# Kernel tuning notes

Hardware: AMD Instinct MI355X
Metric: run time of the kernel (lower is better)

## Reference

```python
import jax, jax.numpy as jnp
import numpy as np

N = 10000      # nodes
E = 65536      # edges
IN = 16        # in_channels
H = 64         # hidden_channels
ED = 4         # edge_attr_dim
MLP_H = 64     # hidden width of edge-weight MLPs


def _glorot(key, shape):
    fan_in, fan_out = shape[0], shape[1]
    lim = np.sqrt(6.0 / (fan_in + fan_out)).astype(np.float32)
    return jax.random.uniform(key, shape, jnp.float32, -lim, lim)


def setup_inputs() -> dict:
    key = jax.random.key(0)
    ks = jax.random.split(key, 16)
    x = jax.random.normal(ks[0], (N, IN), dtype=jnp.float32)
    edge_index = jax.random.randint(ks[1], (2, E), 0, N, dtype=jnp.int64)
    edge_attr = jax.random.normal(ks[2], (E, ED), dtype=jnp.float32)
    return {
        "x": x,
        "edge_index": edge_index,
        "edge_attr": edge_attr,
        # nn1: Linear(ED,64) -> ReLU -> Linear(64, IN*H)
        "nn1_w1": _glorot(ks[3], (ED, MLP_H)), "nn1_b1": jnp.zeros((MLP_H,), jnp.float32),
        "nn1_w2": _glorot(ks[4], (MLP_H, IN * H)), "nn1_b2": jnp.zeros((IN * H,), jnp.float32),
        "root1": _glorot(ks[5], (IN, H)), "bias1": jnp.zeros((H,), jnp.float32),
        # nn2: Linear(ED,64) -> ReLU -> Linear(64, H*H)
        "nn2_w1": _glorot(ks[6], (ED, MLP_H)), "nn2_b1": jnp.zeros((MLP_H,), jnp.float32),
        "nn2_w2": _glorot(ks[7], (MLP_H, H * H)), "nn2_b2": jnp.zeros((H * H,), jnp.float32),
        "root2": _glorot(ks[8], (H, H)), "bias2": jnp.zeros((H,), jnp.float32),
        # readout MLP
        "lin1_w": _glorot(ks[9], (H, 8)), "lin1_b": jnp.zeros((8,), jnp.float32),
        "lin2_w": _glorot(ks[10], (8, 1)), "lin2_b": jnp.zeros((1,), jnp.float32),
    }


def _nnconv(x, src, dst, edge_attr, w1, b1, w2, b2, root, bias, cin, cout):
    # Edge-conditioned weight generation: MLP(edge_attr) -> [E, cin, cout]
    h = jax.nn.relu(edge_attr @ w1 + b1)
    We = (h @ w2 + b2).reshape(-1, cin, cout)
    # Per-edge matmul: message_e = x[src_e] @ We_e  -> [E, cout]
    msg = jnp.einsum('ei,eio->eo', x[src], We)
    # Scatter mean over destination nodes
    s = jax.ops.segment_sum(msg, dst, num_segments=N)
    cnt = jax.ops.segment_sum(jnp.ones((msg.shape[0],), x.dtype), dst, num_segments=N)
    agg = s / jnp.maximum(cnt, 1.0)[:, None]
    # Root transform + bias (PyG NNConv defaults: root_weight=True, bias=True)
    return agg + x @ root + bias


def reference(x, edge_index, edge_attr,
              nn1_w1, nn1_b1, nn1_w2, nn1_b2, root1, bias1,
              nn2_w1, nn2_b1, nn2_w2, nn2_b2, root2, bias2,
              lin1_w, lin1_b, lin2_w, lin2_b):
    # Dropout layers are identity in eval mode.
    src, dst = edge_index[0], edge_index[1]
    h = jax.nn.relu(_nnconv(x, src, dst, edge_attr,
                            nn1_w1, nn1_b1, nn1_w2, nn1_b2, root1, bias1, IN, H))
    h = jax.nn.relu(_nnconv(h, src, dst, edge_attr,
                            nn2_w1, nn2_b1, nn2_w2, nn2_b2, root2, bias2, H, H))
    h = jax.nn.relu(h @ lin1_w + lin1_b)
    return (h @ lin2_w + lin2_b)[:, 0]  # squeeze(-1) -> [N]
```

## Files before the change

kernel.cpp:

```cpp
#include <hip/hip_runtime.h>
#include <hip/hip_bf16.h>

#define NN 10000
#define EE 65536

using short8  = __attribute__((ext_vector_type(8))) short;
using u16x8   = __attribute__((ext_vector_type(8))) unsigned short;
using float4v = __attribute__((ext_vector_type(4))) float;

__device__ __forceinline__ unsigned short f2b(float f){
  union { float f; unsigned int u; } v; v.f = f;
  unsigned int u = v.u;
  unsigned int r = (u + 0x7fff + ((u >> 16) & 1)) >> 16;
  return (unsigned short)r;
}


__device__ __forceinline__ void do_permB(int idx, const float* __restrict__ w2,
                                         unsigned short* __restrict__ Bt, int cin){
  int K = cin*64;
  int o = idx / K;
  int k = idx - o*K;
  int m = k / cin;
  int i = k - m*cin;
  Bt[idx] = f2b(w2[(size_t)m*(cin*64) + i*64 + o]);
}

__global__ __launch_bounds__(256) void k_prep(
    const float* __restrict__ w2a, unsigned short* __restrict__ Bt1,
    const float* __restrict__ w2b, unsigned short* __restrict__ Bt2,
    int* __restrict__ cnt){
  int b = blockIdx.x;
  int t = threadIdx.x;
  if(b < 40){
    int i = b*256 + t;
    if(i < NN) cnt[i] = 0;
  } else if(b < 296){
    do_permB((b-40)*256 + t, w2a, Bt1, 16);
  } else {
    do_permB((b-296)*256 + t, w2b, Bt2, 64);
  }
}


__global__ void k_hist(const int* __restrict__ dst, int* __restrict__ cnt){
  int e = blockIdx.x*256 + threadIdx.x;
  if(e < EE) atomicAdd(&cnt[dst[e]], 1);
}

__global__ __launch_bounds__(1024) void k_scan(const int* __restrict__ cnt, int* __restrict__ offs, int* __restrict__ cursor){
  const int T = 1024, PER = (NN + T - 1)/T;
  int tid = threadIdx.x;
  int base = tid*PER;
  int local[PER];
  int s = 0;
  #pragma unroll
  for(int j=0;j<PER;j++){
    int i = base+j;
    int v = (i<NN)? cnt[i] : 0;
    local[j] = s;
    s += v;
  }
  int lane = tid & 63, wv = tid >> 6;
  int val = s;
  #pragma unroll
  for(int o=1;o<64;o<<=1){
    int u = __shfl_up(val, o, 64);
    if(lane >= o) val += u;
  }
  __shared__ int wsum[16];
  if(lane==63) wsum[wv] = val;
  __syncthreads();
  if(tid==0){
    int acc=0;
    #pragma unroll
    for(int i=0;i<16;i++){ int t2=wsum[i]; wsum[i]=acc; acc+=t2; }
  }
  __syncthreads();
  int thr_excl = wsum[wv] + (val - s);
  #pragma unroll
  for(int j=0;j<PER;j++){
    int i = base+j;
    if(i<NN){ int e = thr_excl + local[j]; offs[i]=e; cursor[i]=e; }
  }
  if(tid == T-1) offs[NN] = thr_excl + s;
}

__global__ void k_scatter(const int* __restrict__ dst, const int* __restrict__ src,
                          int* __restrict__ cursor, int2* __restrict__ elist2){
  int e = blockIdx.x*256 + threadIdx.x;
  if(e < EE){ int p = atomicAdd(&cursor[dst[e]], 1); elist2[p] = make_int2(e, src[e]); }
}


__global__ __launch_bounds__(64) void k_accK1(const float* __restrict__ x,
    const int* __restrict__ offs, const int2* __restrict__ elist2,
    const float* __restrict__ ea, const float* __restrict__ w1, const float* __restrict__ b1,
    unsigned short* __restrict__ K1, float* __restrict__ XS, int v0){
  int v = v0 + blockIdx.x;
  int L = threadIdx.x;
  int cg = L & 3, mg = L >> 2;
  int i0 = cg << 2;
  float w1c0 = w1[L], w1c1 = w1[64+L], w1c2 = w1[128+L], w1c3 = w1[192+L];
  float b1c = b1[L];
  __shared__ float sh[2][64];
  float acc[4][4];
  #pragma unroll
  for(int j=0;j<4;j++)
    #pragma unroll
    for(int c=0;c<4;c++) acc[j][c]=0.f;
  float4 xs = make_float4(0.f,0.f,0.f,0.f);
  int p0 = offs[v], p1 = offs[v+1];
  float4 a_nxt = make_float4(0.f,0.f,0.f,0.f);
  float4 x_nxt = make_float4(0.f,0.f,0.f,0.f);
  if(p0 < p1){
    int2 es = elist2[p0];
    a_nxt = *(const float4*)(ea + (size_t)es.x*4);
    x_nxt = *(const float4*)(x + (size_t)es.y*16 + i0);
  }
  for(int p=p0;p<p1;p++){
    int buf = (p-p0)&1;
    float4 xv = x_nxt;
    float4 av = a_nxt;
    float hv = fmaxf(b1c + av.x*w1c0 + av.y*w1c1 + av.z*w1c2 + av.w*w1c3, 0.f);
    sh[buf][L] = hv;
    __syncthreads();
    if(p+1<p1){
      int2 es = elist2[p+1];
      a_nxt = *(const float4*)(ea + (size_t)es.x*4);
      x_nxt = *(const float4*)(x + (size_t)es.y*16 + i0);
    }
    xs.x += xv.x; xs.y += xv.y; xs.z += xv.z; xs.w += xv.w;
    #pragma unroll
    for(int j=0;j<4;j++){
      float hm = sh[buf][mg + 16*j];
      acc[j][0] += hm*xv.x; acc[j][1] += hm*xv.y;
      acc[j][2] += hm*xv.z; acc[j][3] += hm*xv.w;
    }
  }
  unsigned short* Kv = K1 + (size_t)blockIdx.x*1024;
  #pragma unroll
  for(int j=0;j<4;j++){
    int m = mg + 16*j;
    ushort4 u;
    u.x=f2b(acc[j][0]); u.y=f2b(acc[j][1]); u.z=f2b(acc[j][2]); u.w=f2b(acc[j][3]);
    *(ushort4*)(Kv + m*16 + i0) = u;
  }
  if(mg==0) *(float4*)(XS + (size_t)v*64 + i0) = xs;
}


__global__ __launch_bounds__(64) void k_accK2(const float* __restrict__ x1,
    const int* __restrict__ offs, const int2* __restrict__ elist2,
    const float* __restrict__ ea, const float* __restrict__ w1, const float* __restrict__ b1,
    unsigned short* __restrict__ K, float* __restrict__ XS, int v0){
  int v = v0 + blockIdx.x;
  int L = threadIdx.x;
  int cg = L & 7, mg = L >> 3;
  int i0 = cg << 3;
  float w1c0 = w1[L], w1c1 = w1[64+L], w1c2 = w1[128+L], w1c3 = w1[192+L];
  float b1c = b1[L];
  __shared__ float sh[2][64];
  float acc[8][8];
  #pragma unroll
  for(int j=0;j<8;j++)
    #pragma unroll
    for(int c=0;c<8;c++) acc[j][c]=0.f;
  float4 xs0 = make_float4(0.f,0.f,0.f,0.f);
  float4 xs1 = make_float4(0.f,0.f,0.f,0.f);
  int p0 = offs[v], p1 = offs[v+1];
  float4 a_nxt = make_float4(0.f,0.f,0.f,0.f);
  float4 x_nxt0 = make_float4(0.f,0.f,0.f,0.f);
  float4 x_nxt1 = make_float4(0.f,0.f,0.f,0.f);
  if(p0 < p1){
    int2 es = elist2[p0];
    a_nxt = *(const float4*)(ea + (size_t)es.x*4);
    const float* xr = x1 + (size_t)es.y*64 + i0;
    x_nxt0 = *(const float4*)xr;
    x_nxt1 = *(const float4*)(xr+4);
  }
  for(int p=p0;p<p1;p++){
    int buf = (p-p0)&1;
    float4 xv0 = x_nxt0, xv1 = x_nxt1;
    float4 av = a_nxt;
    float hv = fmaxf(b1c + av.x*w1c0 + av.y*w1c1 + av.z*w1c2 + av.w*w1c3, 0.f);
    sh[buf][L] = hv;
    __syncthreads();
    if(p+1<p1){
      int2 es = elist2[p+1];
      a_nxt = *(const float4*)(ea + (size_t)es.x*4);
      const float* xr = x1 + (size_t)es.y*64 + i0;
      x_nxt0 = *(const float4*)xr;
      x_nxt1 = *(const float4*)(xr+4);
    }
    xs0.x += xv0.x; xs0.y += xv0.y; xs0.z += xv0.z; xs0.w += xv0.w;
    xs1.x += xv1.x; xs1.y += xv1.y; xs1.z += xv1.z; xs1.w += xv1.w;
    float4 h4a = *(float4*)&sh[buf][mg*8];
    float4 h4b = *(float4*)&sh[buf][mg*8+4];
    #pragma unroll
    for(int jj=0;jj<2;jj++){
      float4 h4 = jj? h4b : h4a;
      #pragma unroll
      for(int tq=0;tq<4;tq++){
        int j = jj*4+tq;
        float hm = (tq==0)?h4.x:(tq==1)?h4.y:(tq==2)?h4.z:h4.w;
        acc[j][0] += hm*xv0.x; acc[j][1] += hm*xv0.y;
        acc[j][2] += hm*xv0.z; acc[j][3] += hm*xv0.w;
        acc[j][4] += hm*xv1.x; acc[j][5] += hm*xv1.y;
        acc[j][6] += hm*xv1.z; acc[j][7] += hm*xv1.w;
      }
    }
  }
  unsigned short* Kv = K + (size_t)blockIdx.x*4096;
  #pragma unroll
  for(int j=0;j<8;j++){
    int m = mg*8 + j;
    u16x8 u;
    #pragma unroll
    for(int c=0;c<8;c++) u[c] = f2b(acc[j][c]);
    *(u16x8*)(Kv + m*64 + i0) = u;
  }
  if(mg==0){
    *(float4*)(XS + (size_t)v*64 + i0)     = xs0;
    *(float4*)(XS + (size_t)v*64 + i0 + 4) = xs1;
  }
}


#define GBK 64

__global__ __launch_bounds__(256) void k_gemm(const unsigned short* __restrict__ A,
    const unsigned short* __restrict__ Bt, float* __restrict__ P,
    int rows, int Ktot, int Kc){
  __shared__ unsigned short As[64*72];
  __shared__ unsigned short Bs[64*72];
  int t = threadIdx.x;
  int lane = t & 63;
  int w = t >> 6;
  int row0 = blockIdx.x*64;
  int k0 = blockIdx.y*Kc;

  int srow  = t >> 3;
  int skseg = (t & 7) << 3;

  float4v acc[4];
  #pragma unroll
  for(int ct=0;ct<4;ct++)
    #pragma unroll
    for(int qq=0;qq<4;qq++) acc[ct][qq]=0.f;

  int lrow = lane & 15;
  int lk   = (lane >> 4) << 3;

  short8 a_pf[2], b_pf[2];
  int T = Kc/GBK;

  {
    int kk = k0 + skseg;
    #pragma unroll
    for(int qq=0;qq<2;qq++){
      int gr = row0 + srow + 32*qq;
      short8 z = {0,0,0,0,0,0,0,0};
      a_pf[qq] = (gr<rows)? *(const short8*)(A + (size_t)gr*Ktot + kk) : z;
      int o = srow + 32*qq;
      b_pf[qq] = *(const short8*)(Bt + (size_t)o*Ktot + kk);
    }
  }

  for(int tt=0; tt<T; tt++){
    __syncthreads();
    #pragma unroll
    for(int qq=0;qq<2;qq++){
      *(short8*)(As + (srow + 32*qq)*72 + skseg) = a_pf[qq];
      *(short8*)(Bs + (srow + 32*qq)*72 + skseg) = b_pf[qq];
    }
    __syncthreads();
    if(tt+1 < T){
      int kk = k0 + (tt+1)*GBK + skseg;
      #pragma unroll
      for(int qq=0;qq<2;qq++){
        int gr = row0 + srow + 32*qq;
        short8 z = {0,0,0,0,0,0,0,0};
        a_pf[qq] = (gr<rows)? *(const short8*)(A + (size_t)gr*Ktot + kk) : z;
        int o = srow + 32*qq;
        b_pf[qq] = *(const short8*)(Bt + (size_t)o*Ktot + kk);
      }
    }
    #pragma unroll
    for(int k32=0;k32<2;k32++){
      int kf = k32*32 + lk;
      short8 a0 = *(short8*)(As + (w*16 + lrow)*72 + kf);
      #pragma unroll
      for(int ct=0;ct<4;ct++){
        short8 b = *(short8*)(Bs + (ct*16 + lrow)*72 + kf);
        acc[ct] = __builtin_amdgcn_mfma_f32_16x16x32_bf16(a0, b, acc[ct], 0,0,0);
      }
    }
  }
  size_t base = (size_t)blockIdx.y*rows*64;
  int quad = lane >> 4;
  #pragma unroll
  for(int ct=0;ct<4;ct++){
    int c = ct*16 + lrow;
    #pragma unroll
    for(int reg=0;reg<4;reg++){
      int r = row0 + w*16 + quad*4 + reg;
      if(r < rows) P[base + (size_t)r*64 + c] = acc[ct][reg];
    }
  }
}


template<int CIN, int SPLIT>
__global__ __launch_bounds__(256) void k_reduce_ep(const float* __restrict__ P, int rows, int v0,
    const float* __restrict__ XS, const float* __restrict__ b2, const float* __restrict__ xprev,
    const float* __restrict__ root, const float* __restrict__ bias, const int* __restrict__ offs,
    float* __restrict__ out){
  int idx = blockIdx.x*256 + threadIdx.x;
  if(idx >= rows*16) return;
  int r = idx >> 4, og = (idx & 15) << 2;
  int v = v0 + r;

  float4 s = make_float4(0.f,0.f,0.f,0.f);
  #pragma unroll
  for(int z=0; z<SPLIT; z++){
    float4 p = *(const float4*)(P + ((size_t)z*rows + r)*64 + og);
    s.x += p.x; s.y += p.y; s.z += p.z; s.w += p.w;
  }
  #pragma unroll
  for(int i=0;i<CIN;i++){
    float xsv = XS[(size_t)v*64 + i];
    float4 b = *(const float4*)(b2 + i*64 + og);
    s.x += xsv*b.x; s.y += xsv*b.y; s.z += xsv*b.z; s.w += xsv*b.w;
  }
  float4 rt = make_float4(0.f,0.f,0.f,0.f);
  #pragma unroll
  for(int i=0;i<CIN;i++){
    float xv = xprev[(size_t)v*CIN + i];
    float4 wv = *(const float4*)(root + i*64 + og);
    rt.x += xv*wv.x; rt.y += xv*wv.y; rt.z += xv*wv.z; rt.w += xv*wv.w;
  }
  float c = (float)(offs[v+1]-offs[v]); c = fmaxf(c, 1.f);
  float inv = 1.f/c;
  float4 bi = *(const float4*)(bias + og);
  float4 o;
  o.x = fmaxf(s.x*inv + rt.x + bi.x, 0.f);
  o.y = fmaxf(s.y*inv + rt.y + bi.y, 0.f);
  o.z = fmaxf(s.z*inv + rt.z + bi.z, 0.f);
  o.w = fmaxf(s.w*inv + rt.w + bi.w, 0.f);
  *(float4*)(out + (size_t)v*64 + og) = o;
}


template<int SPLIT>
__global__ __launch_bounds__(256) void k_red2_ro(const float* __restrict__ P, int rows,
    const float* __restrict__ XS, const float* __restrict__ b2, const float* __restrict__ x1,
    const float* __restrict__ root, const float* __restrict__ bias, const int* __restrict__ offs,
    const float* __restrict__ lw1, const float* __restrict__ lb1,
    const float* __restrict__ lw2, const float* __restrict__ lb2,
    float* __restrict__ out){
  __shared__ float row[16][68];
  __shared__ float hjs[16][8];
  int tid = threadIdx.x;
  int idx = blockIdx.x*256 + tid;
  int r = idx >> 4, og = (idx & 15) << 2;
  int n = tid >> 4;
  int nbase = blockIdx.x*16;
  int ninblk = rows - nbase; if(ninblk > 16) ninblk = 16;

  float4 o = make_float4(0.f,0.f,0.f,0.f);
  if(r < rows){
    float4 s = make_float4(0.f,0.f,0.f,0.f);
    #pragma unroll
    for(int z=0; z<SPLIT; z++){
      float4 p = *(const float4*)(P + ((size_t)z*rows + r)*64 + og);
      s.x += p.x; s.y += p.y; s.z += p.z; s.w += p.w;
    }
    #pragma unroll
    for(int i=0;i<64;i++){
      float xsv = XS[(size_t)r*64 + i];
      float4 b = *(const float4*)(b2 + i*64 + og);
      s.x += xsv*b.x; s.y += xsv*b.y; s.z += xsv*b.z; s.w += xsv*b.w;
    }
    float4 rt = make_float4(0.f,0.f,0.f,0.f);
    #pragma unroll
    for(int i=0;i<64;i++){
      float xv = x1[(size_t)r*64 + i];
      float4 wv = *(const float4*)(root + i*64 + og);
      rt.x += xv*wv.x; rt.y += xv*wv.y; rt.z += xv*wv.z; rt.w += xv*wv.w;
    }
    float c = (float)(offs[r+1]-offs[r]); c = fmaxf(c, 1.f);
    float inv = 1.f/c;
    float4 bi = *(const float4*)(bias + og);
    o.x = fmaxf(s.x*inv + rt.x + bi.x, 0.f);
    o.y = fmaxf(s.y*inv + rt.y + bi.y, 0.f);
    o.z = fmaxf(s.z*inv + rt.z + bi.z, 0.f);
    o.w = fmaxf(s.w*inv + rt.w + bi.w, 0.f);
  }
  *(float4*)&row[n][og] = o;
  __syncthreads();
  if(tid < 128){
    int n2 = tid >> 3, j = tid & 7;
    if(n2 < ninblk){
      float a = lb1[j];
      #pragma unroll
      for(int i=0;i<64;i++) a += row[n2][i]*lw1[i*8+j];
      hjs[n2][j] = fmaxf(a, 0.f)*lw2[j];
    }
  }
  __syncthreads();
  if(tid < 16 && tid < ninblk){
    float s = lb2[0];
    #pragma unroll
    for(int j=0;j<8;j++) s += hjs[tid][j];
    out[nbase + tid] = s;
  }
}


__global__ void k_readout(const float* __restrict__ x2, const float* __restrict__ lw1,
                          const float* __restrict__ lb1, const float* __restrict__ lw2,
                          const float* __restrict__ lb2, float* __restrict__ out){
  int v = blockIdx.x*256 + threadIdx.x;
  if(v >= NN) return;
  float accj[8];
  #pragma unroll
  for(int j=0;j<8;j++) accj[j] = lb1[j];
  const float* xr = x2 + (size_t)v*64;
  #pragma unroll 16
  for(int i=0;i<64;i++){
    float xv = xr[i];
    #pragma unroll
    for(int j=0;j<8;j++) accj[j] += xv*lw1[i*8+j];
  }
  float o = lb2[0];
  #pragma unroll
  for(int j=0;j<8;j++) o += fmaxf(accj[j],0.f)*lw2[j];
  out[v] = o;
}


extern "C" void kernel_launch(void* const* d_in, const int* in_sizes, int n_in,
                              void* d_out, int out_size, void* d_ws, size_t ws_size,
                              hipStream_t stream) {
  const float* x      = (const float*)d_in[0];
  const int*   ei     = (const int*)d_in[1];
  const float* ea     = (const float*)d_in[2];
  const float* nn1_w1 = (const float*)d_in[3];
  const float* nn1_b1 = (const float*)d_in[4];
  const float* nn1_w2 = (const float*)d_in[5];
  const float* nn1_b2 = (const float*)d_in[6];
  const float* root1  = (const float*)d_in[7];
  const float* bias1  = (const float*)d_in[8];
  const float* nn2_w1 = (const float*)d_in[9];
  const float* nn2_b1 = (const float*)d_in[10];
  const float* nn2_w2 = (const float*)d_in[11];
  const float* nn2_b2 = (const float*)d_in[12];
  const float* root2  = (const float*)d_in[13];
  const float* bias2  = (const float*)d_in[14];
  const float* lin1_w = (const float*)d_in[15];
  const float* lin1_b = (const float*)d_in[16];
  const float* lin2_w = (const float*)d_in[17];
  const float* lin2_b = (const float*)d_in[18];
  float* out = (float*)d_out;

  const int* srcIdx = ei;
  const int* dstIdx = ei + EE;

  char* w = (char*)d_ws;
  size_t off = 0;
  auto alloc = [&](size_t bytes)->void*{
    void* p = w + off;
    off = (off + bytes + 255) & ~(size_t)255;
    return p;
  };
  int*            cnt    = (int*)           alloc((size_t)NN*4);
  int*            offs   = (int*)           alloc((size_t)(NN+1)*4);
  int*            cursor = (int*)           alloc((size_t)NN*4);
  int2*           elist2 = (int2*)          alloc((size_t)EE*8);
  float*          XS     = (float*)         alloc((size_t)NN*64*4);
  float*          x1     = (float*)         alloc((size_t)NN*64*4);
  unsigned short* Bt1    = (unsigned short*)alloc((size_t)64*1024*2);
  unsigned short* Bt2    = (unsigned short*)alloc((size_t)64*4096*2);
  size_t fixedBytes = off;
  size_t R = (ws_size > fixedBytes) ? (ws_size - fixedBytes) : 0;

  const int S1 = 4, S2 = 8;
  size_t needSingle = (size_t)NN*4096*2 + (size_t)S2*NN*64*4;
  bool single = (R >= needSingle + 4096);

  k_prep   <<<1320, 256, 0, stream>>>(nn1_w2, Bt1, nn2_w2, Bt2, cnt);
  k_hist   <<<(EE+255)/256, 256, 0, stream>>>(dstIdx, cnt);
  k_scan   <<<1, 1024, 0, stream>>>(cnt, offs, cursor);
  k_scatter<<<(EE+255)/256, 256, 0, stream>>>(dstIdx, srcIdx, cursor, elist2);

  if(single){
    unsigned short* Kbuf = (unsigned short*)(w + off);
    float* P = (float*)(w + off + (size_t)NN*4096*2);

    k_accK1<<<NN, 64, 0, stream>>>(x, offs, elist2, ea, nn1_w1, nn1_b1, Kbuf, XS, 0);
    {
      dim3 g((NN+63)/64, S1);
      k_gemm<<<g, 256, 0, stream>>>(Kbuf, Bt1, P, NN, 1024, 1024/S1);
    }
    k_reduce_ep<16,S1><<<(NN*16+255)/256, 256, 0, stream>>>(P, NN, 0, XS, nn1_b2, x,
                                                             root1, bias1, offs, x1);
    k_accK2<<<NN, 64, 0, stream>>>(x1, offs, elist2, ea, nn2_w1, nn2_b1, Kbuf, XS, 0);
    {
      dim3 g((NN+63)/64, S2);
      k_gemm<<<g, 256, 0, stream>>>(Kbuf, Bt2, P, NN, 4096, 4096/S2);
    }
    k_red2_ro<S2><<<(NN+15)/16, 256, 0, stream>>>(P, NN, XS, nn2_b2, x1, root2, bias2, offs,
                                                   lin1_w, lin1_b, lin2_w, lin2_b, out);
  } else {
    float* x2b = (float*)alloc((size_t)NN*64*4);
    R = (ws_size > off) ? (ws_size - off) : 0;
    long long C2 = (long long)(R / (4096*2 + S2*64*4));
    long long C1 = (long long)(R / (1024*2 + S1*64*4));
    if(C2 > NN) C2 = NN; if(C1 > NN) C1 = NN;
    if(C2 < 128) C2 = 128; if(C1 < 128) C1 = 128;
    unsigned short* Kbuf = (unsigned short*)(w + off);
    {
      float* P = (float*)(w + off + (size_t)C1*1024*2);
      for(long long v0=0; v0<NN; v0+=C1){
        int rows = (int)((NN - v0 < C1) ? (NN - v0) : C1);
        k_accK1<<<rows, 64, 0, stream>>>(x, offs, elist2, ea, nn1_w1, nn1_b1, Kbuf, XS, (int)v0);
        dim3 g((rows+63)/64, S1);
        k_gemm<<<g, 256, 0, stream>>>(Kbuf, Bt1, P, rows, 1024, 1024/S1);
        k_reduce_ep<16,S1><<<(rows*16+255)/256, 256, 0, stream>>>(P, rows, (int)v0, XS, nn1_b2, x,
                                                                   root1, bias1, offs, x1);
      }
    }
    {
      float* P = (float*)(w + off + (size_t)C2*4096*2);
      for(long long v0=0; v0<NN; v0+=C2){
        int rows = (int)((NN - v0 < C2) ? (NN - v0) : C2);
        k_accK2<<<rows, 64, 0, stream>>>(x1, offs, elist2, ea, nn2_w1, nn2_b1, Kbuf, XS, (int)v0);
        dim3 g((rows+63)/64, S2);
        k_gemm<<<g, 256, 0, stream>>>(Kbuf, Bt2, P, rows, 4096, 4096/S2);
        k_reduce_ep<64,S2><<<(rows*16+255)/256, 256, 0, stream>>>(P, rows, (int)v0, XS, nn2_b2, x1,
                                                                   root2, bias2, offs, x2b);
      }
    }
    k_readout<<<(NN+255)/256, 256, 0, stream>>>(x2b, lin1_w, lin1_b, lin2_w, lin2_b, out);
  }
}
```

Measured before the change: 207.0 us.

## Replace LDS-tiled GEMM with single-wave direct-load MFMA GEMM, reduce split-K

Replaces the 256-thread GEMM, which staged 64x64 tiles in shared memory, with a one-wavefront kernel. Each wave handles 16 rows and loads A and B fragments straight from global memory into MFMA bf16 instructions, with no LDS and no barriers. Split-K for layer 2 drops from 8 to 4, which halves the partial-sum buffer the reduce step has to read. The cost is that B is re-read from global memory by every wave instead of shared through LDS, so the kernel leans on L2/L1 cache for B reuse. Row counts are assumed to be multiples of 16 (the fallback path rounds chunk sizes down to a multiple of 64), and there is no bounds check any more.

```diff
diff --git a/kernel.cpp b/kernel.cpp
--- a/kernel.cpp
+++ b/kernel.cpp
@@ -227,86 +227,40 @@
 }
 
 
-#define GBK 64
-
-__global__ __launch_bounds__(256) void k_gemm(const unsigned short* __restrict__ A,
+template<int T>
+__global__ __launch_bounds__(64) void k_gemm_nl(const unsigned short* __restrict__ A,
     const unsigned short* __restrict__ Bt, float* __restrict__ P,
-    int rows, int Ktot, int Kc){
-  __shared__ unsigned short As[64*72];
-  __shared__ unsigned short Bs[64*72];
-  int t = threadIdx.x;
-  int lane = t & 63;
-  int w = t >> 6;
-  int row0 = blockIdx.x*64;
-  int k0 = blockIdx.y*Kc;
-
-  int srow  = t >> 3;
-  int skseg = (t & 7) << 3;
-
-  float4v acc[4];
-  #pragma unroll
-  for(int ct=0;ct<4;ct++)
-    #pragma unroll
-    for(int qq=0;qq<4;qq++) acc[ct][qq]=0.f;
-
+    int rows, int Ktot){
+  int lane = threadIdx.x;
+  int rg = blockIdx.x;
+  int k0 = blockIdx.y * (T*32);
   int lrow = lane & 15;
   int lk   = (lane >> 4) << 3;
-
-  short8 a_pf[2], b_pf[2];
-  int T = Kc/GBK;
-
-  {
-    int kk = k0 + skseg;
-    #pragma unroll
-    for(int qq=0;qq<2;qq++){
-      int gr = row0 + srow + 32*qq;
-      short8 z = {0,0,0,0,0,0,0,0};
-      a_pf[qq] = (gr<rows)? *(const short8*)(A + (size_t)gr*Ktot + kk) : z;
-      int o = srow + 32*qq;
-      b_pf[qq] = *(const short8*)(Bt + (size_t)o*Ktot + kk);
-    }
-  }
-
-  for(int tt=0; tt<T; tt++){
-    __syncthreads();
-    #pragma unroll
-    for(int qq=0;qq<2;qq++){
-      *(short8*)(As + (srow + 32*qq)*72 + skseg) = a_pf[qq];
-      *(short8*)(Bs + (srow + 32*qq)*72 + skseg) = b_pf[qq];
-    }
-    __syncthreads();
-    if(tt+1 < T){
-      int kk = k0 + (tt+1)*GBK + skseg;
-      #pragma unroll
-      for(int qq=0;qq<2;qq++){
-        int gr = row0 + srow + 32*qq;
-        short8 z = {0,0,0,0,0,0,0,0};
-        a_pf[qq] = (gr<rows)? *(const short8*)(A + (size_t)gr*Ktot + kk) : z;
-        int o = srow + 32*qq;
-        b_pf[qq] = *(const short8*)(Bt + (size_t)o*Ktot + kk);
-      }
-    }
-    #pragma unroll
-    for(int k32=0;k32<2;k32++){
-      int kf = k32*32 + lk;
-      short8 a0 = *(short8*)(As + (w*16 + lrow)*72 + kf);
-      #pragma unroll
-      for(int ct=0;ct<4;ct++){
-        short8 b = *(short8*)(Bs + (ct*16 + lrow)*72 + kf);
-        acc[ct] = __builtin_amdgcn_mfma_f32_16x16x32_bf16(a0, b, acc[ct], 0,0,0);
-      }
-    }
-  }
-  size_t base = (size_t)blockIdx.y*rows*64;
+  const unsigned short* Ap  = A  + (size_t)(rg*16 + lrow)*Ktot + k0 + lk;
+  const unsigned short* Bp  = Bt + (size_t)lrow*Ktot + k0 + lk;
+  size_t bstep = (size_t)16*Ktot;
+
+  float4v acc0{}, acc1{}, acc2{}, acc3{};
+  #pragma unroll 4
+  for(int t=0; t<T; t++){
+    short8 a  = *(const short8*)(Ap + t*32);
+    short8 b0 = *(const short8*)(Bp + t*32);
+    short8 b1 = *(const short8*)(Bp + bstep   + t*32);
+    short8 b2 = *(const short8*)(Bp + bstep*2 + t*32);
+    short8 b3 = *(const short8*)(Bp + bstep*3 + t*32);
+    acc0 = __builtin_amdgcn_mfma_f32_16x16x32_bf16(a, b0, acc0, 0,0,0);
+    acc1 = __builtin_amdgcn_mfma_f32_16x16x32_bf16(a, b1, acc1, 0,0,0);
+    acc2 = __builtin_amdgcn_mfma_f32_16x16x32_bf16(a, b2, acc2, 0,0,0);
+    acc3 = __builtin_amdgcn_mfma_f32_16x16x32_bf16(a, b3, acc3, 0,0,0);
+  }
   int quad = lane >> 4;
-  #pragma unroll
-  for(int ct=0;ct<4;ct++){
-    int c = ct*16 + lrow;
-    #pragma unroll
-    for(int reg=0;reg<4;reg++){
-      int r = row0 + w*16 + quad*4 + reg;
-      if(r < rows) P[base + (size_t)r*64 + c] = acc[ct][reg];
-    }
+  float* Pr = P + (size_t)blockIdx.y*rows*64 + (size_t)(rg*16 + quad*4)*64 + lrow;
+  #pragma unroll
+  for(int reg=0; reg<4; reg++){
+    Pr[(size_t)reg*64 +  0] = acc0[reg];
+    Pr[(size_t)reg*64 + 16] = acc1[reg];
+    Pr[(size_t)reg*64 + 32] = acc2[reg];
+    Pr[(size_t)reg*64 + 48] = acc3[reg];
   }
 }
 
@@ -485,7 +439,7 @@
   size_t fixedBytes = off;
   size_t R = (ws_size > fixedBytes) ? (ws_size - fixedBytes) : 0;
 
-  const int S1 = 4, S2 = 8;
+  const int S1 = 4, S2 = 4;
   size_t needSingle = (size_t)NN*4096*2 + (size_t)S2*NN*64*4;
   bool single = (R >= needSingle + 4096);
 
@@ -500,15 +454,15 @@
 
     k_accK1<<<NN, 64, 0, stream>>>(x, offs, elist2, ea, nn1_w1, nn1_b1, Kbuf, XS, 0);
     {
-      dim3 g((NN+63)/64, S1);
-      k_gemm<<<g, 256, 0, stream>>>(Kbuf, Bt1, P, NN, 1024, 1024/S1);
+      dim3 g(NN/16, S1);
+      k_gemm_nl<8><<<g, 64, 0, stream>>>(Kbuf, Bt1, P, NN, 1024);
     }
     k_reduce_ep<16,S1><<<(NN*16+255)/256, 256, 0, stream>>>(P, NN, 0, XS, nn1_b2, x,
                                                              root1, bias1, offs, x1);
     k_accK2<<<NN, 64, 0, stream>>>(x1, offs, elist2, ea, nn2_w1, nn2_b1, Kbuf, XS, 0);
     {
-      dim3 g((NN+63)/64, S2);
-      k_gemm<<<g, 256, 0, stream>>>(Kbuf, Bt2, P, NN, 4096, 4096/S2);
+      dim3 g(NN/16, S2);
+      k_gemm_nl<32><<<g, 64, 0, stream>>>(Kbuf, Bt2, P, NN, 4096);
     }
     k_red2_ro<S2><<<(NN+15)/16, 256, 0, stream>>>(P, NN, XS, nn2_b2, x1, root2, bias2, offs,
                                                    lin1_w, lin1_b, lin2_w, lin2_b, out);
@@ -518,6 +472,7 @@
     long long C2 = (long long)(R / (4096*2 + S2*64*4));
     long long C1 = (long long)(R / (1024*2 + S1*64*4));
     if(C2 > NN) C2 = NN; if(C1 > NN) C1 = NN;
+    C2 &= ~63LL; C1 &= ~63LL;
     if(C2 < 128) C2 = 128; if(C1 < 128) C1 = 128;
     unsigned short* Kbuf = (unsigned short*)(w + off);
     {
@@ -525,8 +480,8 @@
       for(long long v0=0; v0<NN; v0+=C1){
         int rows = (int)((NN - v0 < C1) ? (NN - v0) : C1);
         k_accK1<<<rows, 64, 0, stream>>>(x, offs, elist2, ea, nn1_w1, nn1_b1, Kbuf, XS, (int)v0);
-        dim3 g((rows+63)/64, S1);
-        k_gemm<<<g, 256, 0, stream>>>(Kbuf, Bt1, P, rows, 1024, 1024/S1);
+        dim3 g(rows/16, S1);
+        k_gemm_nl<8><<<g, 64, 0, stream>>>(Kbuf, Bt1, P, rows, 1024);
         k_reduce_ep<16,S1><<<(rows*16+255)/256, 256, 0, stream>>>(P, rows, (int)v0, XS, nn1_b2, x,
                                                                    root1, bias1, offs, x1);
       }
@@ -536,8 +491,8 @@
       for(long long v0=0; v0<NN; v0+=C2){
         int rows = (int)((NN - v0 < C2) ? (NN - v0) : C2);
         k_accK2<<<rows, 64, 0, stream>>>(x1, offs, elist2, ea, nn2_w1, nn2_b1, Kbuf, XS, (int)v0);
-        dim3 g((rows+63)/64, S2);
-        k_gemm<<<g, 256, 0, stream>>>(Kbuf, Bt2, P, rows, 4096, 4096/S2);
+        dim3 g(rows/16, S2);
+        k_gemm_nl<32><<<g, 64, 0, stream>>>(Kbuf, Bt2, P, rows, 4096);
         k_reduce_ep<64,S2><<<(rows*16+255)/256, 256, 0, stream>>>(P, rows, (int)v0, XS, nn2_b2, x1,
                                                                    root2, bias2, offs, x2b);
       }
```

After: 236.8 us. 1.14x slower.
